# Optimization experiments

Hardware: AMD Instinct MI355X
Metric: run time of the kernel (lower is better)

## Reference

```python
import jax, jax.numpy as jnp
import numpy as np

B, T, F = 1024, 512, 64
H1, H2, D1, D2, NOUT = 32, 16, 16, 8, 1


def setup_inputs() -> dict:
    key = jax.random.key(0)
    ks = jax.random.split(key, 14)
    s = lambda k, shape, fan: jax.random.normal(k, shape, jnp.float32) / np.sqrt(fan)
    return {
        "x": jax.random.normal(ks[0], (B, T, F), jnp.float32),
        "Wx1": s(ks[1], (F, H1), F),
        "Wh1": s(ks[2], (H1, H1), H1),
        "b1": jnp.zeros((H1,), jnp.float32),
        "Wx2": s(ks[3], (H1, H2), H1),
        "Wh2": s(ks[4], (H2, H2), H2),
        "b2": jnp.zeros((H2,), jnp.float32),
        "W3": s(ks[5], (H2, D1), H2),
        "b3": jnp.zeros((D1,), jnp.float32),
        "W4": s(ks[6], (D1, D2), D1),
        "b4": jnp.zeros((D2,), jnp.float32),
        "Wo": s(ks[7], (D2, NOUT), D2),
        "bo": jnp.zeros((NOUT,), jnp.float32),
    }


def reference(x, Wx1, Wh1, b1, Wx2, Wh2, b2, W3, b3, W4, b4, Wo, bo):
    b = x.shape[0]
    # SimpleRNN 1 (return_sequences=True): h_t = tanh(x_t Wx + h_{t-1} Wh + b)
    # Precompute input projection for all timesteps: [T, B, H1]
    xp1 = jnp.swapaxes(jnp.einsum('btf,fh->bth', x, Wx1) + b1, 0, 1)

    def step1(h, xt):
        h = jnp.tanh(xt + h @ Wh1)
        return h, h

    _, seq1 = jax.lax.scan(step1, jnp.zeros((b, Wh1.shape[0]), x.dtype), xp1)
    # SimpleRNN 2 (return_sequences=False): keep only final state
    xp2 = seq1 @ Wx2 + b2  # [T, B, H2]

    def step2(h, xt):
        h = jnp.tanh(xt + h @ Wh2)
        return h, None

    h2, _ = jax.lax.scan(step2, jnp.zeros((b, Wh2.shape[0]), x.dtype), xp2)
    # Dense head
    y = jax.nn.relu(h2 @ W3 + b3)
    y = y @ W4 + b4
    return y @ Wo + bo
```

## Files before the change

### kernel.cpp

```cpp
#include <hip/hip_runtime.h>

#define BB 1024
#define TB 512
#define FB 64
#define NH1 32
#define NH2 16
#define ND1 16
#define ND2 8

#define WAVE_FENCE() __builtin_amdgcn_fence(__ATOMIC_ACQ_REL, "wavefront")

__device__ __forceinline__ float tanh_fast(float v) {
    float e = __expf(2.0f * v);
    return fmaf(-2.0f, __builtin_amdgcn_rcpf(e + 1.0f), 1.0f);
}

__global__ __attribute__((amdgpu_flat_work_group_size(64, 64)))
           __attribute__((amdgpu_waves_per_eu(1, 1)))
void rnn_fused_kernel(
    const float* __restrict__ x,
    const float* __restrict__ Wx1, const float* __restrict__ Wh1, const float* __restrict__ b1,
    const float* __restrict__ Wx2, const float* __restrict__ Wh2, const float* __restrict__ b2,
    const float* __restrict__ W3,  const float* __restrict__ b3,
    const float* __restrict__ W4,  const float* __restrict__ b4,
    const float* __restrict__ Wo,  const float* __restrict__ bo,
    float* __restrict__ out)
{
    __shared__ __align__(16) float xs[2][FB];
    __shared__ __align__(16) float h1s[NH1];
    __shared__ __align__(16) float h2s[NH2];
    __shared__ __align__(16) float ys[ND1];

    const int lane = threadIdx.x;
    const int h = lane & 31;
    const int p = lane >> 5;
    const int g = lane & 15;
    const int q = lane >> 4;
    const int b = blockIdx.x;

    auto w1 = [&](int i) { return Wx1[(32 * p + i) * NH1 + h]; };
    auto r1 = [&](int i) { return Wh1[(16 * p + i) * NH1 + h]; };
    auto w2 = [&](int i) { return Wx2[(8 * q + i) * NH2 + g]; };
    auto r2 = [&](int i) { return Wh2[(4 * q + i) * NH2 + g]; };
    const float4 wxa = make_float4(w1(0),  w1(1),  w1(2),  w1(3));
    const float4 wxb = make_float4(w1(4),  w1(5),  w1(6),  w1(7));
    const float4 wxc = make_float4(w1(8),  w1(9),  w1(10), w1(11));
    const float4 wxd = make_float4(w1(12), w1(13), w1(14), w1(15));
    const float4 wxe = make_float4(w1(16), w1(17), w1(18), w1(19));
    const float4 wxf = make_float4(w1(20), w1(21), w1(22), w1(23));
    const float4 wxg = make_float4(w1(24), w1(25), w1(26), w1(27));
    const float4 wxh = make_float4(w1(28), w1(29), w1(30), w1(31));
    const float4 wha = make_float4(r1(0),  r1(1),  r1(2),  r1(3));
    const float4 whb = make_float4(r1(4),  r1(5),  r1(6),  r1(7));
    const float4 whc = make_float4(r1(8),  r1(9),  r1(10), r1(11));
    const float4 whd = make_float4(r1(12), r1(13), r1(14), r1(15));
    const float4 x2a = make_float4(w2(0), w2(1), w2(2), w2(3));
    const float4 x2b = make_float4(w2(4), w2(5), w2(6), w2(7));
    const float4 h2w = make_float4(r2(0), r2(1), r2(2), r2(3));
    const float b1v = (p == 0) ? b1[h] : 0.0f;
    const float b2v = (q == 0) ? b2[g] : 0.0f;

    if (lane < NH1) h1s[lane] = 0.0f;
    if (lane < NH2) h2s[lane] = 0.0f;

    const float* xb = x + (size_t)b * TB * FB + lane;
    float xq0 = xb[0 * FB];
    float xq1 = xb[1 * FB];
    float xq2 = xb[2 * FB];
    float xq3 = xb[3 * FB];
    xs[0][lane] = xq0;
    __syncthreads();

#define STEP(T, SLOT, QSTAGE, QREFILL)                                         \
    {                                                                          \
        WAVE_FENCE();            \
        const int t_ = (T);                                                    \
        int tn_ = t_ + 4; tn_ = (tn_ < TB) ? tn_ : (TB - 1);                   \
        const float xnew_ = xb[tn_ * FB];                                      \
        xs[(SLOT) ^ 1][lane] = QSTAGE;                                         \
        float4 hva = *(const float4*)&h1s[16 * p + 0];                         \
        float4 hvb = *(const float4*)&h1s[16 * p + 4];                         \
        float4 hvc = *(const float4*)&h1s[16 * p + 8];                         \
        float4 hvd = *(const float4*)&h1s[16 * p + 12];                        \
        const float4* xv = (const float4*)&xs[SLOT][32 * p];                   \
        float a0 = b1v, a1 = 0.0f, a2 = 0.0f, a3 = 0.0f;                       \
        float4 v_;                                                             \
        v_ = xv[0]; a0 = fmaf(v_.x, wxa.x, a0); a1 = fmaf(v_.y, wxa.y, a1);    \
                    a2 = fmaf(v_.z, wxa.z, a2); a3 = fmaf(v_.w, wxa.w, a3);    \
        v_ = xv[1]; a0 = fmaf(v_.x, wxb.x, a0); a1 = fmaf(v_.y, wxb.y, a1);    \
                    a2 = fmaf(v_.z, wxb.z, a2); a3 = fmaf(v_.w, wxb.w, a3);    \
        v_ = xv[2]; a0 = fmaf(v_.x, wxc.x, a0); a1 = fmaf(v_.y, wxc.y, a1);    \
                    a2 = fmaf(v_.z, wxc.z, a2); a3 = fmaf(v_.w, wxc.w, a3);    \
        v_ = xv[3]; a0 = fmaf(v_.x, wxd.x, a0); a1 = fmaf(v_.y, wxd.y, a1);    \
                    a2 = fmaf(v_.z, wxd.z, a2); a3 = fmaf(v_.w, wxd.w, a3);    \
        v_ = xv[4]; a0 = fmaf(v_.x, wxe.x, a0); a1 = fmaf(v_.y, wxe.y, a1);    \
                    a2 = fmaf(v_.z, wxe.z, a2); a3 = fmaf(v_.w, wxe.w, a3);    \
        v_ = xv[5]; a0 = fmaf(v_.x, wxf.x, a0); a1 = fmaf(v_.y, wxf.y, a1);    \
                    a2 = fmaf(v_.z, wxf.z, a2); a3 = fmaf(v_.w, wxf.w, a3);    \
        v_ = xv[6]; a0 = fmaf(v_.x, wxg.x, a0); a1 = fmaf(v_.y, wxg.y, a1);    \
                    a2 = fmaf(v_.z, wxg.z, a2); a3 = fmaf(v_.w, wxg.w, a3);    \
        v_ = xv[7]; a0 = fmaf(v_.x, wxh.x, a0); a1 = fmaf(v_.y, wxh.y, a1);    \
                    a2 = fmaf(v_.z, wxh.z, a2); a3 = fmaf(v_.w, wxh.w, a3);    \
        a0 = fmaf(hva.x, wha.x, a0); a1 = fmaf(hva.y, wha.y, a1);              \
        a2 = fmaf(hva.z, wha.z, a2); a3 = fmaf(hva.w, wha.w, a3);              \
        a0 = fmaf(hvb.x, whb.x, a0); a1 = fmaf(hvb.y, whb.y, a1);              \
        a2 = fmaf(hvb.z, whb.z, a2); a3 = fmaf(hvb.w, whb.w, a3);              \
        a0 = fmaf(hvc.x, whc.x, a0); a1 = fmaf(hvc.y, whc.y, a1);              \
        a2 = fmaf(hvc.z, whc.z, a2); a3 = fmaf(hvc.w, whc.w, a3);              \
        a0 = fmaf(hvd.x, whd.x, a0); a1 = fmaf(hvd.y, whd.y, a1);              \
        a2 = fmaf(hvd.z, whd.z, a2); a3 = fmaf(hvd.w, whd.w, a3);              \
        float acc = (a0 + a1) + (a2 + a3);                                     \
        acc += __shfl_xor(acc, 32, 64);                                        \
        float h1new = tanh_fast(acc);                                          \
        if (t_ > 0) {    \
            float4 u0 = *(const float4*)&h1s[8 * q + 0];                       \
            float4 u1 = *(const float4*)&h1s[8 * q + 4];                       \
            float4 hw = *(const float4*)&h2s[4 * q];                           \
            float c0 = b2v, c1 = 0.0f;                                         \
            c0 = fmaf(u0.x, x2a.x, c0); c1 = fmaf(u0.y, x2a.y, c1);            \
            c0 = fmaf(u0.z, x2a.z, c0); c1 = fmaf(u0.w, x2a.w, c1);            \
            c0 = fmaf(u1.x, x2b.x, c0); c1 = fmaf(u1.y, x2b.y, c1);            \
            c0 = fmaf(u1.z, x2b.z, c0); c1 = fmaf(u1.w, x2b.w, c1);            \
            c0 = fmaf(hw.x, h2w.x, c0); c1 = fmaf(hw.y, h2w.y, c1);            \
            c0 = fmaf(hw.z, h2w.z, c0); c1 = fmaf(hw.w, h2w.w, c1);            \
            float cc = c0 + c1;                                                \
            cc += __shfl_xor(cc, 16, 64);                                      \
            cc += __shfl_xor(cc, 32, 64);                                      \
            float h2new = tanh_fast(cc);                                       \
            if (lane < NH2) h2s[lane] = h2new;                                 \
        }                                                                      \
        WAVE_FENCE();       \
        if (p == 0) h1s[h] = h1new;                                            \
        QREFILL = xnew_;                                                       \
    }

    for (int tb = 0; tb < TB; tb += 4) {
        STEP(tb + 0, 0, xq1, xq0);
        STEP(tb + 1, 1, xq2, xq1);
        STEP(tb + 2, 0, xq3, xq2);
        STEP(tb + 3, 1, xq0, xq3);
    }
#undef STEP

    WAVE_FENCE();

    {
        float4 u0 = *(const float4*)&h1s[8 * q + 0];
        float4 u1 = *(const float4*)&h1s[8 * q + 4];
        float4 hw = *(const float4*)&h2s[4 * q];
        float c0 = b2v, c1 = 0.0f;
        c0 = fmaf(u0.x, x2a.x, c0); c1 = fmaf(u0.y, x2a.y, c1);
        c0 = fmaf(u0.z, x2a.z, c0); c1 = fmaf(u0.w, x2a.w, c1);
        c0 = fmaf(u1.x, x2b.x, c0); c1 = fmaf(u1.y, x2b.y, c1);
        c0 = fmaf(u1.z, x2b.z, c0); c1 = fmaf(u1.w, x2b.w, c1);
        c0 = fmaf(hw.x, h2w.x, c0); c1 = fmaf(hw.y, h2w.y, c1);
        c0 = fmaf(hw.z, h2w.z, c0); c1 = fmaf(hw.w, h2w.w, c1);
        float cc = c0 + c1;
        cc += __shfl_xor(cc, 16, 64);
        cc += __shfl_xor(cc, 32, 64);
        float h2fin = tanh_fast(cc);
        WAVE_FENCE();
        if (lane < NH2) h2s[lane] = h2fin;
        WAVE_FENCE();
    }

    float a3h = b3[g];
#pragma unroll
    for (int j = 0; j < 16; ++j) a3h = fmaf(h2s[j], W3[j * ND1 + g], a3h);
    float y1 = fmaxf(a3h, 0.0f);
    WAVE_FENCE();
    if (lane < ND1) ys[lane] = y1;
    WAVE_FENCE();

    const int e = lane & 7;
    float a4 = b4[e];
#pragma unroll
    for (int j = 0; j < 16; ++j) a4 = fmaf(ys[j], W4[j * ND2 + e], a4);

    float yo = a4 * Wo[e];
    yo += __shfl_xor(yo, 1, 64);
    yo += __shfl_xor(yo, 2, 64);
    yo += __shfl_xor(yo, 4, 64);
    if (lane == 0) out[b] = yo + bo[0];
}

extern "C" void kernel_launch(void* const* d_in, const int* in_sizes, int n_in,
                              void* d_out, int out_size, void* d_ws, size_t ws_size,
                              hipStream_t stream) {
    const float* x   = (const float*)d_in[0];
    const float* Wx1 = (const float*)d_in[1];
    const float* Wh1 = (const float*)d_in[2];
    const float* b1  = (const float*)d_in[3];
    const float* Wx2 = (const float*)d_in[4];
    const float* Wh2 = (const float*)d_in[5];
    const float* b2  = (const float*)d_in[6];
    const float* W3  = (const float*)d_in[7];
    const float* b3  = (const float*)d_in[8];
    const float* W4  = (const float*)d_in[9];
    const float* b4  = (const float*)d_in[10];
    const float* Wo  = (const float*)d_in[11];
    const float* bo  = (const float*)d_in[12];
    float* out = (float*)d_out;

    rnn_fused_kernel<<<dim3(BB), dim3(64), 0, stream>>>(
        x, Wx1, Wh1, b1, Wx2, Wh2, b2, W3, b3, W4, b4, Wo, bo, out);
}
```

Before: 364.2 us.

## Split RNN into three-wave producer/consumer pipeline with LDS rings and bpermute

Splits the single-wave fused RNN into three wavefronts per block. One computes the input projection for layer 1, one runs the layer-1 recurrence, and one runs layer 2 plus the dense head. They hand data through LDS ring buffers in 4-step chunks, synchronised by block barriers. The recurrent matvecs now broadcast the hidden state with ds_bpermute instead of LDS reloads, which shortens the serial dependency chain per timestep. The cost is 3x the threads per block, a block-wide barrier every chunk, and extra bpermute traffic.

```diff
diff --git a/kernel.cpp b/kernel.cpp
--- a/kernel.cpp
+++ b/kernel.cpp
@@ -8,6 +8,11 @@
 #define ND1 16
 #define ND2 8
 
+#define RD 16
+#define RDM (RD - 1)
+#define CHUNK 4
+#define NCH (TB / CHUNK)
+
 #define WAVE_FENCE() __builtin_amdgcn_fence(__ATOMIC_ACQ_REL, "wavefront")
 
 __device__ __forceinline__ float tanh_fast(float v) {
@@ -15,9 +20,13 @@
     return fmaf(-2.0f, __builtin_amdgcn_rcpf(e + 1.0f), 1.0f);
 }
 
-__global__ __attribute__((amdgpu_flat_work_group_size(64, 64)))
-           __attribute__((amdgpu_waves_per_eu(1, 1)))
-void rnn_fused_kernel(
+__device__ __forceinline__ float bpermf(int byteAddr, int srcBits) {
+    return __int_as_float(__builtin_amdgcn_ds_bpermute(byteAddr, srcBits));
+}
+
+__global__ __attribute__((amdgpu_flat_work_group_size(192, 192)))
+           __attribute__((amdgpu_waves_per_eu(3)))
+void rnn_pipe_kernel(
     const float* __restrict__ x,
     const float* __restrict__ Wx1, const float* __restrict__ Wh1, const float* __restrict__ b1,
     const float* __restrict__ Wx2, const float* __restrict__ Wh2, const float* __restrict__ b2,
@@ -26,62 +35,47 @@
     const float* __restrict__ Wo,  const float* __restrict__ bo,
     float* __restrict__ out)
 {
-    __shared__ __align__(16) float xs[2][FB];
-    __shared__ __align__(16) float h1s[NH1];
+    __shared__ __align__(16) float xs[4][FB];
+    __shared__ __align__(16) float xpring[RD][NH1];
+    __shared__ __align__(16) float h1ring[RD][NH1];
     __shared__ __align__(16) float h2s[NH2];
     __shared__ __align__(16) float ys[ND1];
 
-    const int lane = threadIdx.x;
+    const int tid  = threadIdx.x;
+    const int wid  = tid >> 6;
+    const int lane = tid & 63;
     const int h = lane & 31;
     const int p = lane >> 5;
     const int g = lane & 15;
     const int q = lane >> 4;
     const int b = blockIdx.x;
 
-    auto w1 = [&](int i) { return Wx1[(32 * p + i) * NH1 + h]; };
-    auto r1 = [&](int i) { return Wh1[(16 * p + i) * NH1 + h]; };
-    auto w2 = [&](int i) { return Wx2[(8 * q + i) * NH2 + g]; };
-    auto r2 = [&](int i) { return Wh2[(4 * q + i) * NH2 + g]; };
-    const float4 wxa = make_float4(w1(0),  w1(1),  w1(2),  w1(3));
-    const float4 wxb = make_float4(w1(4),  w1(5),  w1(6),  w1(7));
-    const float4 wxc = make_float4(w1(8),  w1(9),  w1(10), w1(11));
-    const float4 wxd = make_float4(w1(12), w1(13), w1(14), w1(15));
-    const float4 wxe = make_float4(w1(16), w1(17), w1(18), w1(19));
-    const float4 wxf = make_float4(w1(20), w1(21), w1(22), w1(23));
-    const float4 wxg = make_float4(w1(24), w1(25), w1(26), w1(27));
-    const float4 wxh = make_float4(w1(28), w1(29), w1(30), w1(31));
-    const float4 wha = make_float4(r1(0),  r1(1),  r1(2),  r1(3));
-    const float4 whb = make_float4(r1(4),  r1(5),  r1(6),  r1(7));
-    const float4 whc = make_float4(r1(8),  r1(9),  r1(10), r1(11));
-    const float4 whd = make_float4(r1(12), r1(13), r1(14), r1(15));
-    const float4 x2a = make_float4(w2(0), w2(1), w2(2), w2(3));
-    const float4 x2b = make_float4(w2(4), w2(5), w2(6), w2(7));
-    const float4 h2w = make_float4(r2(0), r2(1), r2(2), r2(3));
-    const float b1v = (p == 0) ? b1[h] : 0.0f;
-    const float b2v = (q == 0) ? b2[g] : 0.0f;
-
-    if (lane < NH1) h1s[lane] = 0.0f;
-    if (lane < NH2) h2s[lane] = 0.0f;
-
-    const float* xb = x + (size_t)b * TB * FB + lane;
-    float xq0 = xb[0 * FB];
-    float xq1 = xb[1 * FB];
-    float xq2 = xb[2 * FB];
-    float xq3 = xb[3 * FB];
-    xs[0][lane] = xq0;
-    __syncthreads();
-
-#define STEP(T, SLOT, QSTAGE, QREFILL)                                         \
+    if (wid == 0) {
+        auto w1 = [&](int i) { return Wx1[(32 * p + i) * NH1 + h]; };
+        const float4 wxa = make_float4(w1(0),  w1(1),  w1(2),  w1(3));
+        const float4 wxb = make_float4(w1(4),  w1(5),  w1(6),  w1(7));
+        const float4 wxc = make_float4(w1(8),  w1(9),  w1(10), w1(11));
+        const float4 wxd = make_float4(w1(12), w1(13), w1(14), w1(15));
+        const float4 wxe = make_float4(w1(16), w1(17), w1(18), w1(19));
+        const float4 wxf = make_float4(w1(20), w1(21), w1(22), w1(23));
+        const float4 wxg = make_float4(w1(24), w1(25), w1(26), w1(27));
+        const float4 wxh = make_float4(w1(28), w1(29), w1(30), w1(31));
+        const float b1v = (p == 0) ? b1[h] : 0.0f;
+
+        const float* xb = x + (size_t)b * TB * FB + lane;
+        float xq0 = xb[0 * FB];
+        float xq1 = xb[1 * FB];
+        float xq2 = xb[2 * FB];
+        float xq3 = xb[3 * FB];
+        xs[0][lane] = xq0;
+
+#define PSTEP(T, SLOT, QSTAGE, QREFILL)                                        \
     {                                                                          \
-        WAVE_FENCE();            \
+        WAVE_FENCE();                                                          \
         const int t_ = (T);                                                    \
         int tn_ = t_ + 4; tn_ = (tn_ < TB) ? tn_ : (TB - 1);                   \
-        const float xnew_ = xb[tn_ * FB];                                      \
-        xs[(SLOT) ^ 1][lane] = QSTAGE;                                         \
-        float4 hva = *(const float4*)&h1s[16 * p + 0];                         \
-        float4 hvb = *(const float4*)&h1s[16 * p + 4];                         \
-        float4 hvc = *(const float4*)&h1s[16 * p + 8];                         \
-        float4 hvd = *(const float4*)&h1s[16 * p + 12];                        \
+        const float xnew_ = xb[(size_t)tn_ * FB];                              \
+        xs[((SLOT) + 1) & 3][lane] = QSTAGE;                                   \
         const float4* xv = (const float4*)&xs[SLOT][32 * p];                   \
         float a0 = b1v, a1 = 0.0f, a2 = 0.0f, a3 = 0.0f;                       \
         float4 v_;                                                             \
@@ -101,87 +95,161 @@
                     a2 = fmaf(v_.z, wxg.z, a2); a3 = fmaf(v_.w, wxg.w, a3);    \
         v_ = xv[7]; a0 = fmaf(v_.x, wxh.x, a0); a1 = fmaf(v_.y, wxh.y, a1);    \
                     a2 = fmaf(v_.z, wxh.z, a2); a3 = fmaf(v_.w, wxh.w, a3);    \
-        a0 = fmaf(hva.x, wha.x, a0); a1 = fmaf(hva.y, wha.y, a1);              \
-        a2 = fmaf(hva.z, wha.z, a2); a3 = fmaf(hva.w, wha.w, a3);              \
-        a0 = fmaf(hvb.x, whb.x, a0); a1 = fmaf(hvb.y, whb.y, a1);              \
-        a2 = fmaf(hvb.z, whb.z, a2); a3 = fmaf(hvb.w, whb.w, a3);              \
-        a0 = fmaf(hvc.x, whc.x, a0); a1 = fmaf(hvc.y, whc.y, a1);              \
-        a2 = fmaf(hvc.z, whc.z, a2); a3 = fmaf(hvc.w, whc.w, a3);              \
-        a0 = fmaf(hvd.x, whd.x, a0); a1 = fmaf(hvd.y, whd.y, a1);              \
-        a2 = fmaf(hvd.z, whd.z, a2); a3 = fmaf(hvd.w, whd.w, a3);              \
         float acc = (a0 + a1) + (a2 + a3);                                     \
         acc += __shfl_xor(acc, 32, 64);                                        \
-        float h1new = tanh_fast(acc);                                          \
-        if (t_ > 0) {    \
-            float4 u0 = *(const float4*)&h1s[8 * q + 0];                       \
-            float4 u1 = *(const float4*)&h1s[8 * q + 4];                       \
-            float4 hw = *(const float4*)&h2s[4 * q];                           \
-            float c0 = b2v, c1 = 0.0f;                                         \
-            c0 = fmaf(u0.x, x2a.x, c0); c1 = fmaf(u0.y, x2a.y, c1);            \
-            c0 = fmaf(u0.z, x2a.z, c0); c1 = fmaf(u0.w, x2a.w, c1);            \
-            c0 = fmaf(u1.x, x2b.x, c0); c1 = fmaf(u1.y, x2b.y, c1);            \
-            c0 = fmaf(u1.z, x2b.z, c0); c1 = fmaf(u1.w, x2b.w, c1);            \
-            c0 = fmaf(hw.x, h2w.x, c0); c1 = fmaf(hw.y, h2w.y, c1);            \
-            c0 = fmaf(hw.z, h2w.z, c0); c1 = fmaf(hw.w, h2w.w, c1);            \
-            float cc = c0 + c1;                                                \
-            cc += __shfl_xor(cc, 16, 64);                                      \
-            cc += __shfl_xor(cc, 32, 64);                                      \
-            float h2new = tanh_fast(cc);                                       \
-            if (lane < NH2) h2s[lane] = h2new;                                 \
-        }                                                                      \
-        WAVE_FENCE();       \
-        if (p == 0) h1s[h] = h1new;                                            \
+        WAVE_FENCE();                                                          \
+        if (p == 0) xpring[t_ & RDM][h] = acc;                                 \
         QREFILL = xnew_;                                                       \
     }
 
-    for (int tb = 0; tb < TB; tb += 4) {
-        STEP(tb + 0, 0, xq1, xq0);
-        STEP(tb + 1, 1, xq2, xq1);
-        STEP(tb + 2, 0, xq3, xq2);
-        STEP(tb + 3, 1, xq0, xq3);
-    }
-#undef STEP
-
-    WAVE_FENCE();
-
-    {
-        float4 u0 = *(const float4*)&h1s[8 * q + 0];
-        float4 u1 = *(const float4*)&h1s[8 * q + 4];
-        float4 hw = *(const float4*)&h2s[4 * q];
-        float c0 = b2v, c1 = 0.0f;
-        c0 = fmaf(u0.x, x2a.x, c0); c1 = fmaf(u0.y, x2a.y, c1);
-        c0 = fmaf(u0.z, x2a.z, c0); c1 = fmaf(u0.w, x2a.w, c1);
-        c0 = fmaf(u1.x, x2b.x, c0); c1 = fmaf(u1.y, x2b.y, c1);
-        c0 = fmaf(u1.z, x2b.z, c0); c1 = fmaf(u1.w, x2b.w, c1);
-        c0 = fmaf(hw.x, h2w.x, c0); c1 = fmaf(hw.y, h2w.y, c1);
-        c0 = fmaf(hw.z, h2w.z, c0); c1 = fmaf(hw.w, h2w.w, c1);
-        float cc = c0 + c1;
-        cc += __shfl_xor(cc, 16, 64);
-        cc += __shfl_xor(cc, 32, 64);
-        float h2fin = tanh_fast(cc);
-        WAVE_FENCE();
-        if (lane < NH2) h2s[lane] = h2fin;
-        WAVE_FENCE();
-    }
-
-    float a3h = b3[g];
+        for (int c = 0; c < NCH + 2; ++c) {
+            if (c < NCH) {
+                const int t0 = c * CHUNK;
+                PSTEP(t0 + 0, 0, xq1, xq0);
+                PSTEP(t0 + 1, 1, xq2, xq1);
+                PSTEP(t0 + 2, 2, xq3, xq2);
+                PSTEP(t0 + 3, 3, xq0, xq3);
+            }
+            __syncthreads();
+        }
+#undef PSTEP
+
+    } else if (wid == 1) {
+        auto r1 = [&](int i) { return Wh1[(16 * p + i) * NH1 + h]; };
+        const float4 wha = make_float4(r1(0),  r1(1),  r1(2),  r1(3));
+        const float4 whb = make_float4(r1(4),  r1(5),  r1(6),  r1(7));
+        const float4 whc = make_float4(r1(8),  r1(9),  r1(10), r1(11));
+        const float4 whd = make_float4(r1(12), r1(13), r1(14), r1(15));
+        const int bpb = 64 * p;
+        float h1prev = 0.0f;
+
+#define L1S(xpv, T)                                                            \
+    {                                                                          \
+        const int hh_ = __float_as_int(h1prev);                                \
+        float a0 = 0.0f, a1 = 0.0f, a2 = 0.0f, a3 = 0.0f;                      \
+        a0 = fmaf(bpermf(bpb +  0, hh_), wha.x, a0);                           \
+        a1 = fmaf(bpermf(bpb +  4, hh_), wha.y, a1);                           \
+        a2 = fmaf(bpermf(bpb +  8, hh_), wha.z, a2);                           \
+        a3 = fmaf(bpermf(bpb + 12, hh_), wha.w, a3);                           \
+        a0 = fmaf(bpermf(bpb + 16, hh_), whb.x, a0);                           \
+        a1 = fmaf(bpermf(bpb + 20, hh_), whb.y, a1);                           \
+        a2 = fmaf(bpermf(bpb + 24, hh_), whb.z, a2);                           \
+        a3 = fmaf(bpermf(bpb + 28, hh_), whb.w, a3);                           \
+        a0 = fmaf(bpermf(bpb + 32, hh_), whc.x, a0);                           \
+        a1 = fmaf(bpermf(bpb + 36, hh_), whc.y, a1);                           \
+        a2 = fmaf(bpermf(bpb + 40, hh_), whc.z, a2);                           \
+        a3 = fmaf(bpermf(bpb + 44, hh_), whc.w, a3);                           \
+        a0 = fmaf(bpermf(bpb + 48, hh_), whd.x, a0);                           \
+        a1 = fmaf(bpermf(bpb + 52, hh_), whd.y, a1);                           \
+        a2 = fmaf(bpermf(bpb + 56, hh_), whd.z, a2);                           \
+        a3 = fmaf(bpermf(bpb + 60, hh_), whd.w, a3);                           \
+        float acc = (a0 + a1) + (a2 + a3);                                     \
+        acc += p ? 0.0f : (xpv);               \
+        acc += __shfl_xor(acc, 32, 64);                                        \
+        h1prev = tanh_fast(acc);                                               \
+        WAVE_FENCE();                                                          \
+        if (p == 0) h1ring[(T) & RDM][h] = h1prev;       \
+        WAVE_FENCE();                                                          \
+    }
+
+        for (int c = 0; c < NCH + 2; ++c) {
+            if (c >= 1 && c <= NCH) {
+                const int t0 = (c - 1) * CHUNK;
+                float xp0 = xpring[(t0 + 0) & RDM][h];
+                float xp1 = xpring[(t0 + 1) & RDM][h];
+                float xp2 = xpring[(t0 + 2) & RDM][h];
+                float xp3 = xpring[(t0 + 3) & RDM][h];
+                L1S(xp0, t0 + 0);
+                L1S(xp1, t0 + 1);
+                L1S(xp2, t0 + 2);
+                L1S(xp3, t0 + 3);
+            }
+            __syncthreads();
+        }
+#undef L1S
+
+    } else {
+        auto w2 = [&](int i) { return Wx2[(8 * q + i) * NH2 + g]; };
+        const float4 x2a = make_float4(w2(0), w2(1), w2(2), w2(3));
+        const float4 x2b = make_float4(w2(4), w2(5), w2(6), w2(7));
+        auto r2 = [&](int i) { return Wh2[i * NH2 + g]; };
+        const float4 wh2a = make_float4(r2(0),  r2(1),  r2(2),  r2(3));
+        const float4 wh2b = make_float4(r2(4),  r2(5),  r2(6),  r2(7));
+        const float4 wh2c = make_float4(r2(8),  r2(9),  r2(10), r2(11));
+        const float4 wh2d = make_float4(r2(12), r2(13), r2(14), r2(15));
+        const float b2v = (q == 0) ? b2[g] : 0.0f;
+        float h2prev = 0.0f;
+
+#define L2S(T)                                                                 \
+    {                                                                          \
+        const float* hr_ = &h1ring[(T) & RDM][8 * q];                          \
+        float4 u0 = *(const float4*)(hr_);                                     \
+        float4 u1 = *(const float4*)(hr_ + 4);                                 \
+        float cu0 = b2v, cu1 = 0.0f;                                           \
+        cu0 = fmaf(u0.x, x2a.x, cu0); cu1 = fmaf(u0.y, x2a.y, cu1);            \
+        cu0 = fmaf(u0.z, x2a.z, cu0); cu1 = fmaf(u0.w, x2a.w, cu1);            \
+        cu0 = fmaf(u1.x, x2b.x, cu0); cu1 = fmaf(u1.y, x2b.y, cu1);            \
+        cu0 = fmaf(u1.z, x2b.z, cu0); cu1 = fmaf(u1.w, x2b.w, cu1);            \
+        float cu = cu0 + cu1;                                                  \
+        cu += __shfl_xor(cu, 16, 64);                                          \
+        cu += __shfl_xor(cu, 32, 64);                                          \
+        const int h2i_ = __float_as_int(h2prev);                               \
+        float c0 = 0.0f, c1 = 0.0f, c2 = 0.0f, c3 = 0.0f;                      \
+        c0 = fmaf(bpermf( 0, h2i_), wh2a.x, c0);                               \
+        c1 = fmaf(bpermf( 4, h2i_), wh2a.y, c1);                               \
+        c2 = fmaf(bpermf( 8, h2i_), wh2a.z, c2);                               \
+        c3 = fmaf(bpermf(12, h2i_), wh2a.w, c3);                               \
+        c0 = fmaf(bpermf(16, h2i_), wh2b.x, c0);                               \
+        c1 = fmaf(bpermf(20, h2i_), wh2b.y, c1);                               \
+        c2 = fmaf(bpermf(24, h2i_), wh2b.z, c2);                               \
+        c3 = fmaf(bpermf(28, h2i_), wh2b.w, c3);                               \
+        c0 = fmaf(bpermf(32, h2i_), wh2c.x, c0);                               \
+        c1 = fmaf(bpermf(36, h2i_), wh2c.y, c1);                               \
+        c2 = fmaf(bpermf(40, h2i_), wh2c.z, c2);                               \
+        c3 = fmaf(bpermf(44, h2i_), wh2c.w, c3);                               \
+        c0 = fmaf(bpermf(48, h2i_), wh2d.x, c0);                               \
+        c1 = fmaf(bpermf(52, h2i_), wh2d.y, c1);                               \
+        c2 = fmaf(bpermf(56, h2i_), wh2d.z, c2);                               \
+        c3 = fmaf(bpermf(60, h2i_), wh2d.w, c3);                               \
+        float ch = (c0 + c1) + (c2 + c3);                                      \
+        h2prev = tanh_fast(cu + ch);                                           \
+    }
+
+        for (int c = 0; c < NCH + 2; ++c) {
+            if (c >= 2) {
+                const int t0 = (c - 2) * CHUNK;
+                L2S(t0 + 0);
+                L2S(t0 + 1);
+                L2S(t0 + 2);
+                L2S(t0 + 3);
+            }
+            __syncthreads();
+        }
+#undef L2S
+
+        WAVE_FENCE();
+        if (lane < NH2) h2s[lane] = h2prev;
+        WAVE_FENCE();
+
+        float a3h = b3[g];
 #pragma unroll
-    for (int j = 0; j < 16; ++j) a3h = fmaf(h2s[j], W3[j * ND1 + g], a3h);
-    float y1 = fmaxf(a3h, 0.0f);
-    WAVE_FENCE();
-    if (lane < ND1) ys[lane] = y1;
-    WAVE_FENCE();
-
-    const int e = lane & 7;
-    float a4 = b4[e];
+        for (int j = 0; j < 16; ++j) a3h = fmaf(h2s[j], W3[j * ND1 + g], a3h);
+        float y1 = fmaxf(a3h, 0.0f);
+        WAVE_FENCE();
+        if (lane < ND1) ys[lane] = y1;
+        WAVE_FENCE();
+
+        const int e = lane & 7;
+        float a4 = b4[e];
 #pragma unroll
-    for (int j = 0; j < 16; ++j) a4 = fmaf(ys[j], W4[j * ND2 + e], a4);
-
-    float yo = a4 * Wo[e];
-    yo += __shfl_xor(yo, 1, 64);
-    yo += __shfl_xor(yo, 2, 64);
-    yo += __shfl_xor(yo, 4, 64);
-    if (lane == 0) out[b] = yo + bo[0];
+        for (int j = 0; j < 16; ++j) a4 = fmaf(ys[j], W4[j * ND2 + e], a4);
+
+        float yo = a4 * Wo[e];
+        yo += __shfl_xor(yo, 1, 64);
+        yo += __shfl_xor(yo, 2, 64);
+        yo += __shfl_xor(yo, 4, 64);
+        if (lane == 0) out[b] = yo + bo[0];
+    }
 }
 
 extern "C" void kernel_launch(void* const* d_in, const int* in_sizes, int n_in,
@@ -202,6 +270,6 @@
     const float* bo  = (const float*)d_in[12];
     float* out = (float*)d_out;
 
-    rnn_fused_kernel<<<dim3(BB), dim3(64), 0, stream>>>(
+    rnn_pipe_kernel<<<dim3(BB), dim3(192), 0, stream>>>(
         x, Wx1, Wh1, b1, Wx2, Wh2, b2, W3, b3, W4, b4, Wo, bo, out);
 }
```

After: 355.4 us. 2.4% less time.

## Split input projection into a parallel GEMM pre-pass before the recurrence

Applied to the files above, without the earlier changes.

Moves the x·Wx1 + b1 projection out of the serial timestep loop into a separate massively parallel kernel that writes xp to workspace. The recurrent kernel then reads only one precomputed value per lane per step, prefetched in registers, which shortens the per-step critical path. In exchange it adds a 64MB workspace write and read plus a second launch, and falls back to the fused kernel if no workspace is available.

```diff
diff --git a/kernel.cpp b/kernel.cpp
--- a/kernel.cpp
+++ b/kernel.cpp
@@ -15,9 +15,188 @@
     return fmaf(-2.0f, __builtin_amdgcn_rcpf(e + 1.0f), 1.0f);
 }
 
+__global__ __attribute__((amdgpu_flat_work_group_size(256, 256)))
+void xp_gemm_kernel(const float* __restrict__ x, const float* __restrict__ Wx1,
+                    const float* __restrict__ b1, float* __restrict__ xp)
+{
+    const int b  = blockIdx.x;
+    const int qd = blockIdx.y;
+    const int h  = threadIdx.x & 31;
+    const int ts = threadIdx.x >> 5;
+
+    float wc[FB];
+#pragma unroll
+    for (int f = 0; f < FB; ++f) wc[f] = Wx1[f * NH1 + h];
+    const float bb = b1[h];
+
+    const float* xr  = x  + (size_t)b * TB * FB  + (size_t)(qd * 128) * FB;
+    float*       xpo = xp + (size_t)b * TB * NH1 + (size_t)(qd * 128) * NH1;
+
+#pragma unroll 4
+    for (int k = 0; k < 16; ++k) {
+        const int tl = k * 8 + ts;
+        const float4* xv = (const float4*)(xr + (size_t)tl * FB);
+        float a0 = bb, a1 = 0.0f, a2 = 0.0f, a3 = 0.0f;
+#pragma unroll
+        for (int j = 0; j < 16; ++j) {
+            float4 v = xv[j];
+            a0 = fmaf(v.x, wc[4 * j + 0], a0);
+            a1 = fmaf(v.y, wc[4 * j + 1], a1);
+            a2 = fmaf(v.z, wc[4 * j + 2], a2);
+            a3 = fmaf(v.w, wc[4 * j + 3], a3);
+        }
+        xpo[(size_t)tl * NH1 + h] = (a0 + a1) + (a2 + a3);
+    }
+}
+
 __global__ __attribute__((amdgpu_flat_work_group_size(64, 64)))
            __attribute__((amdgpu_waves_per_eu(1, 1)))
-void rnn_fused_kernel(
+void rnn_seq_kernel(
+    const float* __restrict__ xp,
+    const float* __restrict__ Wh1,
+    const float* __restrict__ Wx2, const float* __restrict__ Wh2, const float* __restrict__ b2,
+    const float* __restrict__ W3,  const float* __restrict__ b3,
+    const float* __restrict__ W4,  const float* __restrict__ b4,
+    const float* __restrict__ Wo,  const float* __restrict__ bo,
+    float* __restrict__ out)
+{
+    __shared__ __align__(16) float h1s[NH1];
+    __shared__ __align__(16) float h2s[NH2];
+    __shared__ __align__(16) float ys[ND1];
+
+    const int lane = threadIdx.x;
+    const int h = lane & 31;
+    const int p = lane >> 5;
+    const int g = lane & 15;
+    const int q = lane >> 4;
+    const int b = blockIdx.x;
+
+    auto r1 = [&](int i) { return Wh1[(16 * p + i) * NH1 + h]; };
+    const float4 wha = make_float4(r1(0),  r1(1),  r1(2),  r1(3));
+    const float4 whb = make_float4(r1(4),  r1(5),  r1(6),  r1(7));
+    const float4 whc = make_float4(r1(8),  r1(9),  r1(10), r1(11));
+    const float4 whd = make_float4(r1(12), r1(13), r1(14), r1(15));
+    auto w2 = [&](int i) { return Wx2[(8 * q + i) * NH2 + g]; };
+    const float4 x2a = make_float4(w2(0), w2(1), w2(2), w2(3));
+    const float4 x2b = make_float4(w2(4), w2(5), w2(6), w2(7));
+    auto r2 = [&](int i) { return Wh2[(4 * q + i) * NH2 + g]; };
+    const float4 h2w = make_float4(r2(0), r2(1), r2(2), r2(3));
+    const float b2v = (q == 0) ? b2[g] : 0.0f;
+
+    if (lane < NH1) h1s[lane] = 0.0f;
+    if (lane < NH2) h2s[lane] = 0.0f;
+    __syncthreads();
+
+    const float* xpb = xp + (size_t)b * TB * NH1 + lane;
+    float xq0 = xpb[0 * NH1];
+    float xq1 = xpb[2 * NH1];
+    float xq2 = xpb[4 * NH1];
+    float xq3 = xpb[6 * NH1];
+
+#define SSTEP(T_E, PAR, XQ)                                                    \
+    {                                                                          \
+        WAVE_FENCE();                                                          \
+        const int t_ = (T_E);                                                  \
+        float4 hva = *(const float4*)&h1s[16 * p + 0];                         \
+        float4 hvb = *(const float4*)&h1s[16 * p + 4];                         \
+        float4 hvc = *(const float4*)&h1s[16 * p + 8];                         \
+        float4 hvd = *(const float4*)&h1s[16 * p + 12];                        \
+        float a0 = (p == (PAR)) ? (XQ) : 0.0f;                                 \
+        float a1 = 0.0f, a2 = 0.0f, a3 = 0.0f;                                 \
+        a0 = fmaf(hva.x, wha.x, a0); a1 = fmaf(hva.y, wha.y, a1);              \
+        a2 = fmaf(hva.z, wha.z, a2); a3 = fmaf(hva.w, wha.w, a3);              \
+        a0 = fmaf(hvb.x, whb.x, a0); a1 = fmaf(hvb.y, whb.y, a1);              \
+        a2 = fmaf(hvb.z, whb.z, a2); a3 = fmaf(hvb.w, whb.w, a3);              \
+        a0 = fmaf(hvc.x, whc.x, a0); a1 = fmaf(hvc.y, whc.y, a1);              \
+        a2 = fmaf(hvc.z, whc.z, a2); a3 = fmaf(hvc.w, whc.w, a3);              \
+        a0 = fmaf(hvd.x, whd.x, a0); a1 = fmaf(hvd.y, whd.y, a1);              \
+        a2 = fmaf(hvd.z, whd.z, a2); a3 = fmaf(hvd.w, whd.w, a3);              \
+        float acc = (a0 + a1) + (a2 + a3);                                     \
+        acc += __shfl_xor(acc, 32, 64);                                        \
+        float h1new = tanh_fast(acc);                                          \
+        if (t_ > 0) {    \
+            float4 u0 = *(const float4*)&h1s[8 * q + 0];                       \
+            float4 u1 = *(const float4*)&h1s[8 * q + 4];                       \
+            float4 hw = *(const float4*)&h2s[4 * q];                           \
+            float c0 = b2v, c1 = 0.0f;                                         \
+            c0 = fmaf(u0.x, x2a.x, c0); c1 = fmaf(u0.y, x2a.y, c1);            \
+            c0 = fmaf(u0.z, x2a.z, c0); c1 = fmaf(u0.w, x2a.w, c1);            \
+            c0 = fmaf(u1.x, x2b.x, c0); c1 = fmaf(u1.y, x2b.y, c1);            \
+            c0 = fmaf(u1.z, x2b.z, c0); c1 = fmaf(u1.w, x2b.w, c1);            \
+            c0 = fmaf(hw.x, h2w.x, c0); c1 = fmaf(hw.y, h2w.y, c1);            \
+            c0 = fmaf(hw.z, h2w.z, c0); c1 = fmaf(hw.w, h2w.w, c1);            \
+            float cc = c0 + c1;                                                \
+            cc += __shfl_xor(cc, 16, 64);                                      \
+            cc += __shfl_xor(cc, 32, 64);                                      \
+            float h2new = tanh_fast(cc);                                       \
+            if (lane < NH2) h2s[lane] = h2new;                                 \
+        }                                                                      \
+        WAVE_FENCE();       \
+        if (p == 0) h1s[h] = h1new;                                            \
+    }
+
+    for (int tb = 0; tb < TB; tb += 8) {
+        int n0 = tb + 8;  n0 = (n0 <= TB - 2) ? n0 : (TB - 2);
+        int n1 = tb + 10; n1 = (n1 <= TB - 2) ? n1 : (TB - 2);
+        int n2 = tb + 12; n2 = (n2 <= TB - 2) ? n2 : (TB - 2);
+        int n3 = tb + 14; n3 = (n3 <= TB - 2) ? n3 : (TB - 2);
+        float xn0 = xpb[(size_t)n0 * NH1];
+        float xn1 = xpb[(size_t)n1 * NH1];
+        float xn2 = xpb[(size_t)n2 * NH1];
+        float xn3 = xpb[(size_t)n3 * NH1];
+        SSTEP(tb + 0, 0, xq0) SSTEP(tb + 1, 1, xq0)
+        SSTEP(tb + 2, 0, xq1) SSTEP(tb + 3, 1, xq1)
+        SSTEP(tb + 4, 0, xq2) SSTEP(tb + 5, 1, xq2)
+        SSTEP(tb + 6, 0, xq3) SSTEP(tb + 7, 1, xq3)
+        xq0 = xn0; xq1 = xn1; xq2 = xn2; xq3 = xn3;
+    }
+#undef SSTEP
+
+    WAVE_FENCE();
+
+    {
+        float4 u0 = *(const float4*)&h1s[8 * q + 0];
+        float4 u1 = *(const float4*)&h1s[8 * q + 4];
+        float4 hw = *(const float4*)&h2s[4 * q];
+        float c0 = b2v, c1 = 0.0f;
+        c0 = fmaf(u0.x, x2a.x, c0); c1 = fmaf(u0.y, x2a.y, c1);
+        c0 = fmaf(u0.z, x2a.z, c0); c1 = fmaf(u0.w, x2a.w, c1);
+        c0 = fmaf(u1.x, x2b.x, c0); c1 = fmaf(u1.y, x2b.y, c1);
+        c0 = fmaf(u1.z, x2b.z, c0); c1 = fmaf(u1.w, x2b.w, c1);
+        c0 = fmaf(hw.x, h2w.x, c0); c1 = fmaf(hw.y, h2w.y, c1);
+        c0 = fmaf(hw.z, h2w.z, c0); c1 = fmaf(hw.w, h2w.w, c1);
+        float cc = c0 + c1;
+        cc += __shfl_xor(cc, 16, 64);
+        cc += __shfl_xor(cc, 32, 64);
+        float h2fin = tanh_fast(cc);
+        WAVE_FENCE();
+        if (lane < NH2) h2s[lane] = h2fin;
+        WAVE_FENCE();
+    }
+
+    float a3h = b3[g];
+#pragma unroll
+    for (int j = 0; j < 16; ++j) a3h = fmaf(h2s[j], W3[j * ND1 + g], a3h);
+    float y1 = fmaxf(a3h, 0.0f);
+    WAVE_FENCE();
+    if (lane < ND1) ys[lane] = y1;
+    WAVE_FENCE();
+
+    const int e = lane & 7;
+    float a4 = b4[e];
+#pragma unroll
+    for (int j = 0; j < 16; ++j) a4 = fmaf(ys[j], W4[j * ND2 + e], a4);
+
+    float yo = a4 * Wo[e];
+    yo += __shfl_xor(yo, 1, 64);
+    yo += __shfl_xor(yo, 2, 64);
+    yo += __shfl_xor(yo, 4, 64);
+    if (lane == 0) out[b] = yo + bo[0];
+}
+
+__global__ __attribute__((amdgpu_flat_work_group_size(64, 64)))
+           __attribute__((amdgpu_waves_per_eu(1, 1)))
+void rnn_fallback_kernel(
     const float* __restrict__ x,
     const float* __restrict__ Wx1, const float* __restrict__ Wh1, const float* __restrict__ b1,
     const float* __restrict__ Wx2, const float* __restrict__ Wh2, const float* __restrict__ b2,
@@ -71,9 +250,9 @@
     xs[0][lane] = xq0;
     __syncthreads();
 
-#define STEP(T, SLOT, QSTAGE, QREFILL)                                         \
+#define FSTEP(T, SLOT, QSTAGE, QREFILL)                                        \
     {                                                                          \
-        WAVE_FENCE();            \
+        WAVE_FENCE();                                                          \
         const int t_ = (T);                                                    \
         int tn_ = t_ + 4; tn_ = (tn_ < TB) ? tn_ : (TB - 1);                   \
         const float xnew_ = xb[tn_ * FB];                                      \
@@ -112,7 +291,7 @@
         float acc = (a0 + a1) + (a2 + a3);                                     \
         acc += __shfl_xor(acc, 32, 64);                                        \
         float h1new = tanh_fast(acc);                                          \
-        if (t_ > 0) {    \
+        if (t_ > 0) {                                                          \
             float4 u0 = *(const float4*)&h1s[8 * q + 0];                       \
             float4 u1 = *(const float4*)&h1s[8 * q + 4];                       \
             float4 hw = *(const float4*)&h2s[4 * q];                           \
@@ -129,21 +308,20 @@
             float h2new = tanh_fast(cc);                                       \
             if (lane < NH2) h2s[lane] = h2new;                                 \
         }                                                                      \
-        WAVE_FENCE();       \
+        WAVE_FENCE();                                                          \
         if (p == 0) h1s[h] = h1new;                                            \
         QREFILL = xnew_;                                                       \
     }
 
     for (int tb = 0; tb < TB; tb += 4) {
-        STEP(tb + 0, 0, xq1, xq0);
-        STEP(tb + 1, 1, xq2, xq1);
-        STEP(tb + 2, 0, xq3, xq2);
-        STEP(tb + 3, 1, xq0, xq3);
-    }
-#undef STEP
-
-    WAVE_FENCE();
-
+        FSTEP(tb + 0, 0, xq1, xq0);
+        FSTEP(tb + 1, 1, xq2, xq1);
+        FSTEP(tb + 2, 0, xq3, xq2);
+        FSTEP(tb + 3, 1, xq0, xq3);
+    }
+#undef FSTEP
+
+    WAVE_FENCE();
     {
         float4 u0 = *(const float4*)&h1s[8 * q + 0];
         float4 u1 = *(const float4*)&h1s[8 * q + 4];
@@ -202,6 +380,14 @@
     const float* bo  = (const float*)d_in[12];
     float* out = (float*)d_out;
 
-    rnn_fused_kernel<<<dim3(BB), dim3(64), 0, stream>>>(
-        x, Wx1, Wh1, b1, Wx2, Wh2, b2, W3, b3, W4, b4, Wo, bo, out);
-}
+    const size_t need = (size_t)BB * TB * NH1 * sizeof(float);
+    if (d_ws != nullptr && ws_size >= need) {
+        float* xpw = (float*)d_ws;
+        xp_gemm_kernel<<<dim3(BB, 4), dim3(256), 0, stream>>>(x, Wx1, b1, xpw);
+        rnn_seq_kernel<<<dim3(BB), dim3(64), 0, stream>>>(
+            xpw, Wh1, Wx2, Wh2, b2, W3, b3, W4, b4, Wo, bo, out);
+    } else {
+        rnn_fallback_kernel<<<dim3(BB), dim3(64), 0, stream>>>(
+            x, Wx1, Wh1, b1, Wx2, Wh2, b2, W3, b3, W4, b4, Wo, bo, out);
+    }
+}
```

Result: slower. 495.0 us (+35.9%).

## Restructure RNN recurrence with DPP row rotations and role-split wave rows

Applied to the files above, without the earlier changes.

Splits the 64-lane wave into four 16-lane rows with distinct roles: one row computes the layer-1 recurrence, one the layer-2 step, and two compute the input projection for a later timestep. Operands are exchanged within each row through DPP row-rotate instead of LDS float4 broadcasts, with weights pre-permuted into registers to match the rotation. The layers are software-pipelined across timesteps, with epilogue iterations to drain the pipeline. This is meant to cut LDS traffic and shortens the per-step critical path, at the cost of many more weight registers and more intricate timestep bookkeeping.

```diff
diff --git a/kernel.cpp b/kernel.cpp
--- a/kernel.cpp
+++ b/kernel.cpp
@@ -15,9 +15,29 @@
     return fmaf(-2.0f, __builtin_amdgcn_rcpf(e + 1.0f), 1.0f);
 }
 
+#define DPPF(x, N) __int_as_float(__builtin_amdgcn_update_dpp(                 \
+    0, __float_as_int(x), 0x120 + (N), 0xF, 0xF, false))
+
+#define ASTEP0                                                                 \
+    {                                                                          \
+        acc0 = fmaf(frag0, wq0[0], acc0); acc1 = fmaf(frag1, wq1[0], acc1);    \
+        acc2 = fmaf(frag2, wq2[0], acc2); acc3 = fmaf(frag3, wq3[0], acc3);    \
+    }
+#define ASTEP(S)                                                               \
+    {                                                                          \
+        float r0_ = DPPF(frag0, S); float r1_ = DPPF(frag1, S);                \
+        float r2_ = DPPF(frag2, S); float r3_ = DPPF(frag3, S);                \
+        acc0 = fmaf(r0_, wq0[S], acc0); acc1 = fmaf(r1_, wq1[S], acc1);        \
+        acc2 = fmaf(r2_, wq2[S], acc2); acc3 = fmaf(r3_, wq3[S], acc3);        \
+    }
+#define ASTEPS                                                                 \
+    ASTEP0    ASTEP(1)  ASTEP(2)  ASTEP(3)  ASTEP(4)  ASTEP(5)  ASTEP(6)      \
+    ASTEP(7)  ASTEP(8)  ASTEP(9)  ASTEP(10) ASTEP(11) ASTEP(12) ASTEP(13)     \
+    ASTEP(14) ASTEP(15)
+
 __global__ __attribute__((amdgpu_flat_work_group_size(64, 64)))
            __attribute__((amdgpu_waves_per_eu(1, 1)))
-void rnn_fused_kernel(
+void rnn_dpp_kernel(
     const float* __restrict__ x,
     const float* __restrict__ Wx1, const float* __restrict__ Wh1, const float* __restrict__ b1,
     const float* __restrict__ Wx2, const float* __restrict__ Wh2, const float* __restrict__ b2,
@@ -26,156 +46,137 @@
     const float* __restrict__ Wo,  const float* __restrict__ bo,
     float* __restrict__ out)
 {
-    __shared__ __align__(16) float xs[2][FB];
-    __shared__ __align__(16) float h1s[NH1];
-    __shared__ __align__(16) float h2s[NH2];
-    __shared__ __align__(16) float ys[ND1];
+    __shared__ __align__(16) float xpL[2][NH1];
+    __shared__ __align__(16) float h1L[NH1];
+    __shared__ __align__(16) float h2L[NH2];
+    __shared__ __align__(16) float ysL[ND1];
 
     const int lane = threadIdx.x;
-    const int h = lane & 31;
-    const int p = lane >> 5;
+    const int row  = lane >> 4;
+    const int r    = lane & 15;
+    const int b    = blockIdx.x;
+
+    const int pr = __builtin_amdgcn_update_dpp(0, r, 0x121, 0xF, 0xF, false);
+    const int dj = (pr == ((r + 1) & 15)) ? 1 : 15;
+
+    const int h0o = 2 * r, h1o = 2 * r + 1;
+    const int hx  = (row >= 2) ? ((row - 2) * 16 + r) : 0;
+    float wq0[16], wq1[16], wq2[16], wq3[16];
+#pragma unroll
+    for (int s = 0; s < 16; ++s) {
+        const int j = (r + dj * s) & 15;
+        float a0, a1, a2, a3;
+        if (row == 0) {
+            a0 = Wh1[(2 * j) * NH1 + h0o]; a1 = Wh1[(2 * j + 1) * NH1 + h0o];
+            a2 = Wh1[(2 * j) * NH1 + h1o]; a3 = Wh1[(2 * j + 1) * NH1 + h1o];
+        } else if (row == 1) {
+            a0 = Wx2[(2 * j) * NH2 + r];   a1 = Wx2[(2 * j + 1) * NH2 + r];
+            a2 = Wh2[j * NH2 + r];         a3 = 0.0f;
+        } else {
+            a0 = Wx1[(4 * j + 0) * NH1 + hx]; a1 = Wx1[(4 * j + 1) * NH1 + hx];
+            a2 = Wx1[(4 * j + 2) * NH1 + hx]; a3 = Wx1[(4 * j + 3) * NH1 + hx];
+        }
+        wq0[s] = a0; wq1[s] = a1; wq2[s] = a2; wq3[s] = a3;
+    }
+    const float init0 = (row >= 2) ? b1[hx] : ((row == 1) ? b2[r] : 0.0f);
+
+    float frag0 = 0.0f, frag1 = 0.0f, frag2 = 0.0f, frag3 = 0.0f;
+    const float* xB = x + (size_t)b * TB * FB + 4 * r;
+    float4 qA = make_float4(0.f, 0.f, 0.f, 0.f);
+    float4 qB = qA, qC = qA, qD = qA, fnext = qA;
+    if (row >= 2) {
+        float4 f0 = *(const float4*)(xB + 0 * FB);
+        fnext     = *(const float4*)(xB + 1 * FB);
+        qA = *(const float4*)(xB + 2 * FB);
+        qB = *(const float4*)(xB + 3 * FB);
+        qC = *(const float4*)(xB + 4 * FB);
+        qD = *(const float4*)(xB + 5 * FB);
+        frag0 = f0.x; frag1 = f0.y; frag2 = f0.z; frag3 = f0.w;
+    }
+    if (lane < NH1) h1L[lane] = 0.0f;
+    WAVE_FENCE();
+
+    {
+        float acc0 = init0, acc1 = 0.0f, acc2 = 0.0f, acc3 = 0.0f;
+        ASTEPS
+        WAVE_FENCE();
+        if (row >= 2) {
+            xpL[0][hx] = ((acc0 + acc1) + (acc2 + acc3));
+            frag0 = fnext.x; frag1 = fnext.y; frag2 = fnext.z; frag3 = fnext.w;
+        }
+        WAVE_FENCE();
+    }
+
+#define ITER(T_, PAR_, QH_)                                                    \
+    {                                                                          \
+        float acc0 = init0, acc1 = 0.0f, acc2 = 0.0f, acc3 = 0.0f;             \
+        ASTEPS                                                                 \
+        const float S1_ = acc0 + acc1;                                         \
+        const float S2_ = acc2 + acc3;                                         \
+        const float Tv_ = S1_ + S2_;                                           \
+        const float2 xv_ = *(const float2*)&xpL[PAR_][2 * r];                  \
+        const float u0_ = tanh_fast(S1_ + xv_.x);                              \
+        const float u1_ = tanh_fast(S2_ + xv_.y);                              \
+        const float uT_ = tanh_fast(Tv_);                                      \
+        WAVE_FENCE();                                                          \
+        if (row == 1) {         \
+            float2 hp_ = *(const float2*)&h1L[2 * r];                          \
+            frag2 = ((T_) >= 2) ? uT_ : 0.0f;                                  \
+            frag0 = hp_.x; frag1 = hp_.y;                                      \
+        }                                                                      \
+        WAVE_FENCE();                                                          \
+        if (row == 0) {        \
+            *(float2*)&h1L[2 * r] = make_float2(u0_, u1_);                     \
+            frag0 = u0_; frag1 = u1_; frag2 = u0_; frag3 = u1_;                \
+        }                                                                      \
+        if (row >= 2) {   \
+            xpL[(PAR_) ^ 1][hx] = Tv_;                                         \
+            frag0 = QH_.x; frag1 = QH_.y; frag2 = QH_.z; frag3 = QH_.w;        \
+            int tn_ = (T_) + 6; tn_ = (tn_ < TB) ? tn_ : (TB - 1);             \
+            QH_ = *(const float4*)(xB + (size_t)tn_ * FB);                     \
+        }                                                                      \
+        WAVE_FENCE();                                                          \
+    }
+
+#pragma unroll 1
+    for (int t = 0; t < TB; t += 4) {
+        ITER(t + 0, 0, qA)
+        ITER(t + 1, 1, qB)
+        ITER(t + 2, 0, qC)
+        ITER(t + 3, 1, qD)
+    }
+#undef ITER
+
+#pragma unroll 1
+    for (int e = 0; e < 2; ++e) {
+        float acc0 = init0, acc1 = 0.0f, acc2 = 0.0f, acc3 = 0.0f;
+        ASTEPS
+        const float uT_ = tanh_fast((acc0 + acc1) + (acc2 + acc3));
+        WAVE_FENCE();
+        if (row == 1) {
+            float2 hp_ = *(const float2*)&h1L[2 * r];
+            frag2 = uT_;
+            frag0 = hp_.x; frag1 = hp_.y;
+        }
+        WAVE_FENCE();
+    }
+
+    if (row == 1) h2L[r] = frag2;
+    WAVE_FENCE();
+
     const int g = lane & 15;
-    const int q = lane >> 4;
-    const int b = blockIdx.x;
-
-    auto w1 = [&](int i) { return Wx1[(32 * p + i) * NH1 + h]; };
-    auto r1 = [&](int i) { return Wh1[(16 * p + i) * NH1 + h]; };
-    auto w2 = [&](int i) { return Wx2[(8 * q + i) * NH2 + g]; };
-    auto r2 = [&](int i) { return Wh2[(4 * q + i) * NH2 + g]; };
-    const float4 wxa = make_float4(w1(0),  w1(1),  w1(2),  w1(3));
-    const float4 wxb = make_float4(w1(4),  w1(5),  w1(6),  w1(7));
-    const float4 wxc = make_float4(w1(8),  w1(9),  w1(10), w1(11));
-    const float4 wxd = make_float4(w1(12), w1(13), w1(14), w1(15));
-    const float4 wxe = make_float4(w1(16), w1(17), w1(18), w1(19));
-    const float4 wxf = make_float4(w1(20), w1(21), w1(22), w1(23));
-    const float4 wxg = make_float4(w1(24), w1(25), w1(26), w1(27));
-    const float4 wxh = make_float4(w1(28), w1(29), w1(30), w1(31));
-    const float4 wha = make_float4(r1(0),  r1(1),  r1(2),  r1(3));
-    const float4 whb = make_float4(r1(4),  r1(5),  r1(6),  r1(7));
-    const float4 whc = make_float4(r1(8),  r1(9),  r1(10), r1(11));
-    const float4 whd = make_float4(r1(12), r1(13), r1(14), r1(15));
-    const float4 x2a = make_float4(w2(0), w2(1), w2(2), w2(3));
-    const float4 x2b = make_float4(w2(4), w2(5), w2(6), w2(7));
-    const float4 h2w = make_float4(r2(0), r2(1), r2(2), r2(3));
-    const float b1v = (p == 0) ? b1[h] : 0.0f;
-    const float b2v = (q == 0) ? b2[g] : 0.0f;
-
-    if (lane < NH1) h1s[lane] = 0.0f;
-    if (lane < NH2) h2s[lane] = 0.0f;
-
-    const float* xb = x + (size_t)b * TB * FB + lane;
-    float xq0 = xb[0 * FB];
-    float xq1 = xb[1 * FB];
-    float xq2 = xb[2 * FB];
-    float xq3 = xb[3 * FB];
-    xs[0][lane] = xq0;
-    __syncthreads();
-
-#define STEP(T, SLOT, QSTAGE, QREFILL)                                         \
-    {                                                                          \
-        WAVE_FENCE();            \
-        const int t_ = (T);                                                    \
-        int tn_ = t_ + 4; tn_ = (tn_ < TB) ? tn_ : (TB - 1);                   \
-        const float xnew_ = xb[tn_ * FB];                                      \
-        xs[(SLOT) ^ 1][lane] = QSTAGE;                                         \
-        float4 hva = *(const float4*)&h1s[16 * p + 0];                         \
-        float4 hvb = *(const float4*)&h1s[16 * p + 4];                         \
-        float4 hvc = *(const float4*)&h1s[16 * p + 8];                         \
-        float4 hvd = *(const float4*)&h1s[16 * p + 12];                        \
-        const float4* xv = (const float4*)&xs[SLOT][32 * p];                   \
-        float a0 = b1v, a1 = 0.0f, a2 = 0.0f, a3 = 0.0f;                       \
-        float4 v_;                                                             \
-        v_ = xv[0]; a0 = fmaf(v_.x, wxa.x, a0); a1 = fmaf(v_.y, wxa.y, a1);    \
-                    a2 = fmaf(v_.z, wxa.z, a2); a3 = fmaf(v_.w, wxa.w, a3);    \
-        v_ = xv[1]; a0 = fmaf(v_.x, wxb.x, a0); a1 = fmaf(v_.y, wxb.y, a1);    \
-                    a2 = fmaf(v_.z, wxb.z, a2); a3 = fmaf(v_.w, wxb.w, a3);    \
-        v_ = xv[2]; a0 = fmaf(v_.x, wxc.x, a0); a1 = fmaf(v_.y, wxc.y, a1);    \
-                    a2 = fmaf(v_.z, wxc.z, a2); a3 = fmaf(v_.w, wxc.w, a3);    \
-        v_ = xv[3]; a0 = fmaf(v_.x, wxd.x, a0); a1 = fmaf(v_.y, wxd.y, a1);    \
-                    a2 = fmaf(v_.z, wxd.z, a2); a3 = fmaf(v_.w, wxd.w, a3);    \
-        v_ = xv[4]; a0 = fmaf(v_.x, wxe.x, a0); a1 = fmaf(v_.y, wxe.y, a1);    \
-                    a2 = fmaf(v_.z, wxe.z, a2); a3 = fmaf(v_.w, wxe.w, a3);    \
-        v_ = xv[5]; a0 = fmaf(v_.x, wxf.x, a0); a1 = fmaf(v_.y, wxf.y, a1);    \
-                    a2 = fmaf(v_.z, wxf.z, a2); a3 = fmaf(v_.w, wxf.w, a3);    \
-        v_ = xv[6]; a0 = fmaf(v_.x, wxg.x, a0); a1 = fmaf(v_.y, wxg.y, a1);    \
-                    a2 = fmaf(v_.z, wxg.z, a2); a3 = fmaf(v_.w, wxg.w, a3);    \
-        v_ = xv[7]; a0 = fmaf(v_.x, wxh.x, a0); a1 = fmaf(v_.y, wxh.y, a1);    \
-                    a2 = fmaf(v_.z, wxh.z, a2); a3 = fmaf(v_.w, wxh.w, a3);    \
-        a0 = fmaf(hva.x, wha.x, a0); a1 = fmaf(hva.y, wha.y, a1);              \
-        a2 = fmaf(hva.z, wha.z, a2); a3 = fmaf(hva.w, wha.w, a3);              \
-        a0 = fmaf(hvb.x, whb.x, a0); a1 = fmaf(hvb.y, whb.y, a1);              \
-        a2 = fmaf(hvb.z, whb.z, a2); a3 = fmaf(hvb.w, whb.w, a3);              \
-        a0 = fmaf(hvc.x, whc.x, a0); a1 = fmaf(hvc.y, whc.y, a1);              \
-        a2 = fmaf(hvc.z, whc.z, a2); a3 = fmaf(hvc.w, whc.w, a3);              \
-        a0 = fmaf(hvd.x, whd.x, a0); a1 = fmaf(hvd.y, whd.y, a1);              \
-        a2 = fmaf(hvd.z, whd.z, a2); a3 = fmaf(hvd.w, whd.w, a3);              \
-        float acc = (a0 + a1) + (a2 + a3);                                     \
-        acc += __shfl_xor(acc, 32, 64);                                        \
-        float h1new = tanh_fast(acc);                                          \
-        if (t_ > 0) {    \
-            float4 u0 = *(const float4*)&h1s[8 * q + 0];                       \
-            float4 u1 = *(const float4*)&h1s[8 * q + 4];                       \
-            float4 hw = *(const float4*)&h2s[4 * q];                           \
-            float c0 = b2v, c1 = 0.0f;                                         \
-            c0 = fmaf(u0.x, x2a.x, c0); c1 = fmaf(u0.y, x2a.y, c1);            \
-            c0 = fmaf(u0.z, x2a.z, c0); c1 = fmaf(u0.w, x2a.w, c1);            \
-            c0 = fmaf(u1.x, x2b.x, c0); c1 = fmaf(u1.y, x2b.y, c1);            \
-            c0 = fmaf(u1.z, x2b.z, c0); c1 = fmaf(u1.w, x2b.w, c1);            \
-            c0 = fmaf(hw.x, h2w.x, c0); c1 = fmaf(hw.y, h2w.y, c1);            \
-            c0 = fmaf(hw.z, h2w.z, c0); c1 = fmaf(hw.w, h2w.w, c1);            \
-            float cc = c0 + c1;                                                \
-            cc += __shfl_xor(cc, 16, 64);                                      \
-            cc += __shfl_xor(cc, 32, 64);                                      \
-            float h2new = tanh_fast(cc);                                       \
-            if (lane < NH2) h2s[lane] = h2new;                                 \
-        }                                                                      \
-        WAVE_FENCE();       \
-        if (p == 0) h1s[h] = h1new;                                            \
-        QREFILL = xnew_;                                                       \
-    }
-
-    for (int tb = 0; tb < TB; tb += 4) {
-        STEP(tb + 0, 0, xq1, xq0);
-        STEP(tb + 1, 1, xq2, xq1);
-        STEP(tb + 2, 0, xq3, xq2);
-        STEP(tb + 3, 1, xq0, xq3);
-    }
-#undef STEP
-
-    WAVE_FENCE();
-
-    {
-        float4 u0 = *(const float4*)&h1s[8 * q + 0];
-        float4 u1 = *(const float4*)&h1s[8 * q + 4];
-        float4 hw = *(const float4*)&h2s[4 * q];
-        float c0 = b2v, c1 = 0.0f;
-        c0 = fmaf(u0.x, x2a.x, c0); c1 = fmaf(u0.y, x2a.y, c1);
-        c0 = fmaf(u0.z, x2a.z, c0); c1 = fmaf(u0.w, x2a.w, c1);
-        c0 = fmaf(u1.x, x2b.x, c0); c1 = fmaf(u1.y, x2b.y, c1);
-        c0 = fmaf(u1.z, x2b.z, c0); c1 = fmaf(u1.w, x2b.w, c1);
-        c0 = fmaf(hw.x, h2w.x, c0); c1 = fmaf(hw.y, h2w.y, c1);
-        c0 = fmaf(hw.z, h2w.z, c0); c1 = fmaf(hw.w, h2w.w, c1);
-        float cc = c0 + c1;
-        cc += __shfl_xor(cc, 16, 64);
-        cc += __shfl_xor(cc, 32, 64);
-        float h2fin = tanh_fast(cc);
-        WAVE_FENCE();
-        if (lane < NH2) h2s[lane] = h2fin;
-        WAVE_FENCE();
-    }
-
     float a3h = b3[g];
 #pragma unroll
-    for (int j = 0; j < 16; ++j) a3h = fmaf(h2s[j], W3[j * ND1 + g], a3h);
+    for (int j = 0; j < 16; ++j) a3h = fmaf(h2L[j], W3[j * ND1 + g], a3h);
     float y1 = fmaxf(a3h, 0.0f);
     WAVE_FENCE();
-    if (lane < ND1) ys[lane] = y1;
+    if (lane < ND1) ysL[lane] = y1;
     WAVE_FENCE();
 
     const int e = lane & 7;
     float a4 = b4[e];
 #pragma unroll
-    for (int j = 0; j < 16; ++j) a4 = fmaf(ys[j], W4[j * ND2 + e], a4);
+    for (int j = 0; j < 16; ++j) a4 = fmaf(ysL[j], W4[j * ND2 + e], a4);
 
     float yo = a4 * Wo[e];
     yo += __shfl_xor(yo, 1, 64);
@@ -202,6 +203,6 @@
     const float* bo  = (const float*)d_in[12];
     float* out = (float*)d_out;
 
-    rnn_fused_kernel<<<dim3(BB), dim3(64), 0, stream>>>(
+    rnn_dpp_kernel<<<dim3(BB), dim3(64), 0, stream>>>(
         x, Wx1, Wh1, b1, Wx2, Wh2, b2, W3, b3, W4, b4, Wo, bo, out);
 }
```

Result: slower. 580.4 us (+59.4%).
